# Performance work log

Hardware: AMD Instinct MI355X
Metric: run time of the kernel (lower is better)

## Reference

```python
import jax, jax.numpy as jnp
import numpy as np

N_NODES = 100000
N_EDGES = 1600000
IN_CH = 128
HID = 128
OUT_DIM = 1
N_LAYERS = 3
N_GRAPHS = 512


def setup_inputs() -> dict:
    key = jax.random.key(0)
    ks = jax.random.split(key, 12)
    x = jax.random.normal(ks[0], (N_NODES, IN_CH), dtype=jnp.float32)
    edge_index = jax.random.randint(ks[1], (2, N_EDGES), 0, N_NODES, dtype=jnp.int64)
    batch = jnp.sort(jax.random.randint(ks[2], (N_NODES,), 0, N_GRAPHS, dtype=jnp.int64))
    # GCNConv weights (glorot) and biases; layer 0: in->hid, rest hid->hid (all 128x128 here)
    def glorot(k, fan_in, fan_out):
        lim = jnp.sqrt(6.0 / (fan_in + fan_out)).astype(jnp.float32)
        return jax.random.uniform(k, (fan_in, fan_out), jnp.float32, -lim, lim)
    Ws = jnp.stack([glorot(ks[3 + i], IN_CH if i == 0 else HID, HID) for i in range(N_LAYERS)])
    bs = jnp.zeros((N_LAYERS, HID), dtype=jnp.float32)
    head_w = glorot(ks[8], HID, OUT_DIM)  # stored as [hid, out] == head_weight.T
    head_b = jnp.zeros((OUT_DIM,), dtype=jnp.float32)
    return {"x": x, "edge_index": edge_index, "batch": batch,
            "Ws": Ws, "bs": bs, "head_w": head_w, "head_b": head_b}


def _gcn_norm(edge_index, n_nodes):
    # PyG gcn_norm: add self-loops, deg over dst, norm = d^-1/2[src]*d^-1/2[dst]
    loops = jnp.arange(n_nodes, dtype=edge_index.dtype)
    src = jnp.concatenate([edge_index[0], loops])
    dst = jnp.concatenate([edge_index[1], loops])
    deg = jax.ops.segment_sum(jnp.ones_like(dst, dtype=jnp.float32), dst, num_segments=n_nodes)
    dinv = jnp.where(deg > 0, jax.lax.rsqrt(deg), 0.0)
    norm = dinv[src] * dinv[dst]
    return src, dst, norm


def reference(x, edge_index, batch, Ws, bs, head_w, head_b):
    n = x.shape[0]
    src, dst, norm = _gcn_norm(edge_index, n)
    h = x.astype(jnp.float32)
    for i in range(N_LAYERS):
        t = h @ Ws[i]                                   # [N, hid]
        msg = t[src] * norm[:, None]                    # gather + scale [E+N, hid]
        h = jax.ops.segment_sum(msg, dst, num_segments=n) + bs[i]
        h = jax.nn.relu(h)                              # dropout p=0 -> identity
    g = jax.ops.segment_sum(h, batch, num_segments=N_GRAPHS)  # global_add_pool
    out = g @ head_w + head_b                           # [G, 1]
    return out.reshape(-1)                              # squeeze out_dim==1
```

## Files before the change

kernel.cpp:

```cpp
#include <hip/hip_runtime.h>

#define NN 100000
#define NE 1600000
#define CH 128
#define NG 512
#define NL 3
#define BSZ 512
#define NBUK ((NN + BSZ - 1) / BSZ)
#define TILE 4096

typedef short bf8 __attribute__((ext_vector_type(8)));
typedef float f4 __attribute__((ext_vector_type(4)));
typedef unsigned int u32x4 __attribute__((ext_vector_type(4)));
typedef unsigned short u16;
typedef unsigned int u32;

__device__ __forceinline__ long long ld_idx(const void* p, long long i, bool is64) {
    return is64 ? ((const long long*)p)[i] : (long long)((const int*)p)[i];
}
__device__ __forceinline__ u16 f2bf(float f) {
    u32 u = __float_as_uint(f);
    u += 0x7fffu + ((u >> 16) & 1u);
    return (u16)(u >> 16);
}
__device__ __forceinline__ float bflo(u32 v) { return __uint_as_float(v << 16); }
__device__ __forceinline__ float bfhi(u32 v) { return __uint_as_float(v & 0xffff0000u); }

__global__ void k_zero(int* bcnt, int* flags) {
    int i = blockIdx.x * blockDim.x + threadIdx.x;
    if (i < NBUK) bcnt[i] = 0;
    if (i < 2) flags[i] = 0;
}

__global__ void k_detect(const int* __restrict__ ei32, const int* __restrict__ b32, int* flags) {
    int acc_e = 0, acc_b = 0;
    long long stride = (long long)gridDim.x * blockDim.x;
    long long t0 = (long long)blockIdx.x * blockDim.x + threadIdx.x;
    for (long long i = t0; i < (1 << 18); i += stride) acc_e |= ei32[2 * i + 1];
    for (long long i = t0; i < NN / 2; i += stride) acc_b |= b32[2 * i + 1];
    if (acc_e) atomicOr(&flags[0], 1);
    if (acc_b) atomicOr(&flags[1], 1);
}


__global__ __launch_bounds__(256) void k_hist(const void* __restrict__ ei,
                                              const int* __restrict__ flags,
                                              int* __restrict__ bcnt) {
    __shared__ int cnt[NBUK];
    int tid = threadIdx.x;
    long long e0 = (long long)blockIdx.x * TILE;
    bool is64 = (flags[0] == 0);
    for (int b = tid; b < NBUK; b += 256) cnt[b] = 0;
    __syncthreads();
#pragma unroll
    for (int k = 0; k < 16; ++k) {
        long long e = e0 + tid + k * 256;
        if (e < NE) {
            int d = (int)ld_idx(ei, NE + e, is64);
            atomicAdd(&cnt[d >> 9], 1);
        }
    }
    __syncthreads();
    for (int b = tid; b < NBUK; b += 256)
        if (cnt[b]) atomicAdd(&bcnt[b], cnt[b]);
}

__global__ __launch_bounds__(256) void k_bscan(const int* __restrict__ bcnt,
                                               int* __restrict__ gbase,
                                               int* __restrict__ gcur,
                                               int* __restrict__ rowptr) {
    __shared__ int ws4[4];
    int t = threadIdx.x;
    int v = (t < NBUK) ? bcnt[t] : 0;
    int x = v;
#pragma unroll
    for (int d = 1; d < 64; d <<= 1) {
        int y = __shfl_up(x, d, 64);
        if ((t & 63) >= d) x += y;
    }
    if ((t & 63) == 63) ws4[t >> 6] = x;
    __syncthreads();
    if (t == 0) {
        int s = 0;
#pragma unroll
        for (int w = 0; w < 4; ++w) { int tmp = ws4[w]; ws4[w] = s; s += tmp; }
    }
    __syncthreads();
    int ex = x - v + ws4[t >> 6];
    if (t < NBUK) { gbase[t] = ex; gcur[t] = ex; }
    if (t == NBUK - 1) gbase[NBUK] = ex + v;
    if (t == 0) rowptr[NN] = NE;
}

__global__ __launch_bounds__(256) void k_bin(const void* __restrict__ ei,
                                             const int* __restrict__ flags,
                                             int* __restrict__ gcur,
                                             u32* __restrict__ bin) {
    __shared__ u32 stag[TILE];
    __shared__ int cnt[NBUK], loff[NBUK], lcur[NBUK], gb_s[NBUK];
    int tid = threadIdx.x;
    long long e0 = (long long)blockIdx.x * TILE;
    bool is64 = (flags[0] == 0);

    u32 rec[16];
    int bk[16];
#pragma unroll
    for (int k = 0; k < 16; ++k) {
        long long e = e0 + tid + k * 256;
        if (e < NE) {
            int s = (int)ld_idx(ei, e, is64);
            int d = (int)ld_idx(ei, NE + e, is64);
            rec[k] = ((u32)s << 9) | (u32)(d & (BSZ - 1));
            bk[k] = d >> 9;
        } else bk[k] = -1;
    }
    for (int b = tid; b < NBUK; b += 256) { cnt[b] = 0; lcur[b] = 0; }
    __syncthreads();
#pragma unroll
    for (int k = 0; k < 16; ++k)
        if (bk[k] >= 0) atomicAdd(&cnt[bk[k]], 1);
    __syncthreads();
    if (tid == 0) {
        int run = 0;
        for (int b = 0; b < NBUK; ++b) { loff[b] = run; run += cnt[b]; }
    }
    __syncthreads();
    if (tid < NBUK && cnt[tid] > 0) gb_s[tid] = atomicAdd(&gcur[tid], cnt[tid]);
    __syncthreads();
#pragma unroll
    for (int k = 0; k < 16; ++k)
        if (bk[k] >= 0) {
            int pos = loff[bk[k]] + atomicAdd(&lcur[bk[k]], 1);
            stag[pos] = rec[k];
        }
    __syncthreads();
    int wv = tid >> 6, lane = tid & 63;
    for (int b = wv; b < NBUK; b += 4) {
        int n = cnt[b];
        int gb = (n > 0) ? gb_s[b] : 0;
        int lo = loff[b];
        for (int j = lane; j < n; j += 64) bin[gb + j] = stag[lo + j];
    }
}

__global__ __launch_bounds__(512) void k_fillc(const u32* __restrict__ bin,
                                               const int* __restrict__ gbase,
                                               int* __restrict__ rowptr,
                                               float* __restrict__ dinv,
                                               u32* __restrict__ csr) {
    __shared__ int cnt[BSZ];
    __shared__ int lcur[BSZ];
    __shared__ int wsum[8];
    int b = blockIdx.x, tid = threadIdx.x;
    int gb = gbase[b], ge = gbase[b + 1];
    cnt[tid] = 0;
    __syncthreads();
    for (int i = gb + tid; i < ge; i += BSZ)
        atomicAdd(&cnt[bin[i] & (BSZ - 1)], 1);
    __syncthreads();
    int v = cnt[tid];
    int x = v;
#pragma unroll
    for (int d = 1; d < 64; d <<= 1) {
        int y = __shfl_up(x, d, 64);
        if ((tid & 63) >= d) x += y;
    }
    if ((tid & 63) == 63) wsum[tid >> 6] = x;
    __syncthreads();
    if (tid == 0) {
        int s = 0;
#pragma unroll
        for (int w = 0; w < 8; ++w) { int tmp = wsum[w]; wsum[w] = s; s += tmp; }
    }
    __syncthreads();
    int off = gb + x - v + wsum[tid >> 6];
    int node = b * BSZ + tid;
    if (node < NN) {
        rowptr[node] = off;
        dinv[node] = rsqrtf((float)v + 1.0f);
    }
    lcur[tid] = off;
    __syncthreads();
    for (int i = gb + tid; i < ge; i += BSZ) {
        u32 rec = bin[i];
        int pos = atomicAdd(&lcur[rec & (BSZ - 1)], 1);
        csr[pos] = rec >> 9;
    }
}

__global__ void k_cvt(const float* __restrict__ x, u16* __restrict__ xb,
                      const float* __restrict__ Ws, u16* __restrict__ Wt) {
    long long i = ((long long)blockIdx.x * blockDim.x + threadIdx.x) * 4;
    const long long NX = (long long)NN * CH;
    if (i < NX) {
        float4 v = *(const float4*)(x + i);
        ushort4 o;
        o.x = f2bf(v.x); o.y = f2bf(v.y); o.z = f2bf(v.z); o.w = f2bf(v.w);
        *(ushort4*)(xb + i) = o;
    } else {
        int j = (int)(i - NX);
        if (j >= NL * CH * CH) return;
        int l = j >> 14, c = (j >> 7) & 127, k = j & 127;
        ushort4 o;
        o.x = f2bf(Ws[(l << 14) + ((k + 0) << 7) + c]);
        o.y = f2bf(Ws[(l << 14) + ((k + 1) << 7) + c]);
        o.z = f2bf(Ws[(l << 14) + ((k + 2) << 7) + c]);
        o.w = f2bf(Ws[(l << 14) + ((k + 3) << 7) + c]);
        *(ushort4*)(Wt + j) = o;
    }
}

__global__ __launch_bounds__(256) void k_mm(const u16* __restrict__ A,
                                            const u16* __restrict__ Wt,
                                            u16* __restrict__ out) {
    int tid = threadIdx.x;
    int lane = tid & 63;
    int wv = tid >> 6;
    int rbase = blockIdx.x * 128 + wv * 32;
    int lm = lane & 15;
    int lk = (lane >> 4) << 3;

    f4 acc[2][8];
#pragma unroll
    for (int m = 0; m < 2; ++m)
#pragma unroll
        for (int n = 0; n < 8; ++n) acc[m][n] = (f4){0.f, 0.f, 0.f, 0.f};

    int r0 = rbase + lm;      if (r0 >= NN) r0 = NN - 1;
    int r1 = rbase + 16 + lm; if (r1 >= NN) r1 = NN - 1;

#pragma unroll
    for (int kk = 0; kk < 4; ++kk) {
        int ko = kk * 32 + lk;
        bf8 a0 = *(const bf8*)(A + (size_t)r0 * CH + ko);
        bf8 a1 = *(const bf8*)(A + (size_t)r1 * CH + ko);
#pragma unroll
        for (int n = 0; n < 8; ++n) {
            bf8 b = *(const bf8*)(Wt + (n * 16 + lm) * CH + ko);
            acc[0][n] = __builtin_amdgcn_mfma_f32_16x16x32_bf16(a0, b, acc[0][n], 0, 0, 0);
            acc[1][n] = __builtin_amdgcn_mfma_f32_16x16x32_bf16(a1, b, acc[1][n], 0, 0, 0);
        }
    }

#pragma unroll
    for (int m = 0; m < 2; ++m) {
        int rb = rbase + m * 16 + (lane >> 4) * 4;
#pragma unroll
        for (int r = 0; r < 4; ++r) {
            int row = rb + r;
            if (row < NN) {
#pragma unroll
                for (int n = 0; n < 8; ++n)
                    out[(size_t)row * CH + n * 16 + lm] = f2bf(acc[m][n][r]);
            }
        }
    }
}

#define ACC8W(v, w) \
    acc[0] = fmaf(bflo(v[0]), w, acc[0]); acc[1] = fmaf(bfhi(v[0]), w, acc[1]); \
    acc[2] = fmaf(bflo(v[1]), w, acc[2]); acc[3] = fmaf(bfhi(v[1]), w, acc[3]); \
    acc[4] = fmaf(bflo(v[2]), w, acc[4]); acc[5] = fmaf(bfhi(v[2]), w, acc[5]); \
    acc[6] = fmaf(bflo(v[3]), w, acc[6]); acc[7] = fmaf(bfhi(v[3]), w, acc[7]);

__global__ __launch_bounds__(256) void k_aggr(const u16* __restrict__ t,
                                              const int* __restrict__ rowptr,
                                              const u32* __restrict__ csr,
                                              const float* __restrict__ dinv,
                                              const float* __restrict__ b,
                                              u16* __restrict__ h,
                                              const float* __restrict__ hw,
                                              float* __restrict__ partial) {
    int node = blockIdx.x * 16 + (threadIdx.x >> 4);
    if (node >= NN) return;
    int l16 = threadIdx.x & 15;
    int c8 = l16 << 3;
    const u32x4* tp = (const u32x4*)t;

    int beg = rowptr[node], end = rowptr[node + 1];
    float dn = dinv[node];
    float acc[8];
#pragma unroll
    for (int k = 0; k < 8; ++k) acc[k] = 0.f;

    int j = beg;
    for (; j + 4 <= end; j += 4) {
        int s0 = (int)csr[j], s1 = (int)csr[j + 1];
        int s2 = (int)csr[j + 2], s3 = (int)csr[j + 3];
        float w0 = dinv[s0], w1 = dinv[s1], w2 = dinv[s2], w3 = dinv[s3];
        u32x4 v0 = tp[s0 * 16 + l16];
        u32x4 v1 = tp[s1 * 16 + l16];
        u32x4 v2 = tp[s2 * 16 + l16];
        u32x4 v3 = tp[s3 * 16 + l16];
        ACC8W(v0, w0); ACC8W(v1, w1); ACC8W(v2, w2); ACC8W(v3, w3);
    }
    for (; j < end; ++j) {
        int s = (int)csr[j];
        float w = dinv[s];
        u32x4 v = tp[s * 16 + l16];
        ACC8W(v, w);
    }

    u32x4 sv = tp[node * 16 + l16];
    float4 b0 = *(const float4*)(b + c8);
    float4 b1 = *(const float4*)(b + c8 + 4);
    float r[8];
    r[0] = fmaxf(fmaf(fmaf(bflo(sv[0]), dn, acc[0]), dn, b0.x), 0.f);
    r[1] = fmaxf(fmaf(fmaf(bfhi(sv[0]), dn, acc[1]), dn, b0.y), 0.f);
    r[2] = fmaxf(fmaf(fmaf(bflo(sv[1]), dn, acc[2]), dn, b0.z), 0.f);
    r[3] = fmaxf(fmaf(fmaf(bfhi(sv[1]), dn, acc[3]), dn, b0.w), 0.f);
    r[4] = fmaxf(fmaf(fmaf(bflo(sv[2]), dn, acc[4]), dn, b1.x), 0.f);
    r[5] = fmaxf(fmaf(fmaf(bfhi(sv[2]), dn, acc[5]), dn, b1.y), 0.f);
    r[6] = fmaxf(fmaf(fmaf(bflo(sv[3]), dn, acc[6]), dn, b1.z), 0.f);
    r[7] = fmaxf(fmaf(fmaf(bfhi(sv[3]), dn, acc[7]), dn, b1.w), 0.f);

    if (hw) {
        float4 w0 = *(const float4*)(hw + c8);
        float4 w1 = *(const float4*)(hw + c8 + 4);
        float d = r[0] * w0.x + r[1] * w0.y + r[2] * w0.z + r[3] * w0.w
                + r[4] * w1.x + r[5] * w1.y + r[6] * w1.z + r[7] * w1.w;
#pragma unroll
        for (int off = 8; off > 0; off >>= 1) d += __shfl_xor(d, off);
        if (l16 == 0) partial[node] = d;
    } else {
        u32x4 o;
        o[0] = ((u32)f2bf(r[1]) << 16) | (u32)f2bf(r[0]);
        o[1] = ((u32)f2bf(r[3]) << 16) | (u32)f2bf(r[2]);
        o[2] = ((u32)f2bf(r[5]) << 16) | (u32)f2bf(r[4]);
        o[3] = ((u32)f2bf(r[7]) << 16) | (u32)f2bf(r[6]);
        ((u32x4*)h)[node * 16 + l16] = o;
    }
}


__device__ __forceinline__ int lbound(const void* bt, bool is64, int target) {
    int lo = 0, hi = NN;
    while (lo < hi) {
        int mid = (lo + hi) >> 1;
        long long v = ld_idx(bt, mid, is64);
        if (v < (long long)target) lo = mid + 1; else hi = mid;
    }
    return lo;
}

__global__ __launch_bounds__(256) void k_head(const float* __restrict__ partial,
                                              const void* __restrict__ batch,
                                              const int* __restrict__ flags,
                                              const float* __restrict__ hb,
                                              float* __restrict__ out) {
    int g = blockIdx.x * 4 + (threadIdx.x >> 6);
    if (g >= NG) return;
    int lane = threadIdx.x & 63;
    bool is64 = (flags[1] == 0);
    int lo = lbound(batch, is64, g);
    int hi = lbound(batch, is64, g + 1);
    float s = 0.f;
    for (int i = lo + lane; i < hi; i += 64) s += partial[i];
#pragma unroll
    for (int off = 32; off > 0; off >>= 1) s += __shfl_down(s, off);
    if (lane == 0) out[g] = s + hb[0];
}

extern "C" void kernel_launch(void* const* d_in, const int* in_sizes, int n_in,
                              void* d_out, int out_size, void* d_ws, size_t ws_size,
                              hipStream_t stream) {
    const float* x  = (const float*)d_in[0];
    const void*  ei = d_in[1];
    const void*  bt = d_in[2];
    const float* Ws = (const float*)d_in[3];
    const float* bs = (const float*)d_in[4];
    const float* hw = (const float*)d_in[5];
    const float* hb = (const float*)d_in[6];
    float* out = (float*)d_out;

    char* ws = (char*)d_ws;
    size_t p = 0;
    auto alloc = [&](size_t bytes) { size_t r = p; p += (bytes + 255) & ~(size_t)255; return r; };
    size_t o_flags  = alloc(256);
    size_t o_dinv   = alloc((size_t)NN * 4);
    size_t o_rowptr = alloc((size_t)(NN + 1) * 4);
    size_t o_bcnt   = alloc((size_t)NBUK * 4);
    size_t o_gbase  = alloc((size_t)(NBUK + 1) * 4);
    size_t o_gcur   = alloc((size_t)NBUK * 4);
    size_t o_part   = alloc((size_t)NN * 4);
    size_t o_bin    = alloc((size_t)NE * 4);
    size_t o_csr    = alloc((size_t)NE * 4);
    size_t o_xb     = alloc((size_t)NN * CH * 2);
    size_t o_tb     = alloc((size_t)NN * CH * 2);
    size_t o_hb     = alloc((size_t)NN * CH * 2);
    size_t o_wt     = alloc((size_t)NL * CH * CH * 2);
    (void)ws_size;

    int*   flags  = (int*)(ws + o_flags);
    float* dinv   = (float*)(ws + o_dinv);
    int*   rowptr = (int*)(ws + o_rowptr);
    int*   bcnt   = (int*)(ws + o_bcnt);
    int*   gbase  = (int*)(ws + o_gbase);
    int*   gcur   = (int*)(ws + o_gcur);
    float* part   = (float*)(ws + o_part);
    u32*   bin    = (u32*)(ws + o_bin);
    u32*   csr    = (u32*)(ws + o_csr);
    u16*   xb     = (u16*)(ws + o_xb);
    u16*   tb     = (u16*)(ws + o_tb);
    u16*   hbuf   = (u16*)(ws + o_hb);
    u16*   Wt     = (u16*)(ws + o_wt);

    k_zero<<<1, 256, 0, stream>>>(bcnt, flags);
    k_detect<<<256, 256, 0, stream>>>((const int*)ei, (const int*)bt, flags);
    k_hist<<<(NE + TILE - 1) / TILE, 256, 0, stream>>>(ei, flags, bcnt);
    k_bscan<<<1, 256, 0, stream>>>(bcnt, gbase, gcur, rowptr);
    k_bin<<<(NE + TILE - 1) / TILE, 256, 0, stream>>>(ei, flags, gcur, bin);
    k_fillc<<<NBUK, BSZ, 0, stream>>>(bin, gbase, rowptr, dinv, csr);

    long long ncv = (long long)NN * CH / 4 + NL * CH * CH / 4;
    k_cvt<<<(int)((ncv + 255) / 256), 256, 0, stream>>>(x, xb, Ws, Wt);

    const u16* hin = xb;
    for (int l = 0; l < NL; ++l) {
        bool last = (l == NL - 1);
        k_mm<<<(NN + 127) / 128, 256, 0, stream>>>(hin, Wt + (size_t)l * CH * CH, tb);
        k_aggr<<<(NN + 15) / 16, 256, 0, stream>>>(tb, rowptr, csr, dinv,
                                                   bs + (size_t)l * CH, hbuf,
                                                   last ? hw : nullptr, part);
        hin = hbuf;
    }

    k_head<<<(NG + 3) / 4, 256, 0, stream>>>(part, bt, flags, hb, out);
}
```

Measured before the change: 373.2 us.

## Fuse fp32-to-bf16 input conversion into first GEMM and unroll aggregation by 8

The separate conversion pass over x is removed. The first-layer matmul now reads fp32 x directly and converts it to bf16 in registers, which saves writing and re-reading a 25.6 MB bf16 copy. Weight conversion moves to a small separate kernel. The aggregation gather loop also gains an 8-way unrolled stage to keep more independent loads in flight, at the cost of more registers.

```diff
diff --git a/kernel.cpp b/kernel.cpp
--- a/kernel.cpp
+++ b/kernel.cpp
@@ -188,31 +188,22 @@
     }
 }
 
-__global__ void k_cvt(const float* __restrict__ x, u16* __restrict__ xb,
-                      const float* __restrict__ Ws, u16* __restrict__ Wt) {
-    long long i = ((long long)blockIdx.x * blockDim.x + threadIdx.x) * 4;
-    const long long NX = (long long)NN * CH;
-    if (i < NX) {
-        float4 v = *(const float4*)(x + i);
-        ushort4 o;
-        o.x = f2bf(v.x); o.y = f2bf(v.y); o.z = f2bf(v.z); o.w = f2bf(v.w);
-        *(ushort4*)(xb + i) = o;
-    } else {
-        int j = (int)(i - NX);
-        if (j >= NL * CH * CH) return;
-        int l = j >> 14, c = (j >> 7) & 127, k = j & 127;
-        ushort4 o;
-        o.x = f2bf(Ws[(l << 14) + ((k + 0) << 7) + c]);
-        o.y = f2bf(Ws[(l << 14) + ((k + 1) << 7) + c]);
-        o.z = f2bf(Ws[(l << 14) + ((k + 2) << 7) + c]);
-        o.w = f2bf(Ws[(l << 14) + ((k + 3) << 7) + c]);
-        *(ushort4*)(Wt + j) = o;
-    }
-}
-
-__global__ __launch_bounds__(256) void k_mm(const u16* __restrict__ A,
-                                            const u16* __restrict__ Wt,
-                                            u16* __restrict__ out) {
+__global__ void k_cvt_w(const float* __restrict__ Ws, u16* __restrict__ Wt) {
+    int j = (blockIdx.x * blockDim.x + threadIdx.x) * 4;
+    if (j >= NL * CH * CH) return;
+    int l = j >> 14, c = (j >> 7) & 127, k = j & 127;
+    ushort4 o;
+    o.x = f2bf(Ws[(l << 14) + ((k + 0) << 7) + c]);
+    o.y = f2bf(Ws[(l << 14) + ((k + 1) << 7) + c]);
+    o.z = f2bf(Ws[(l << 14) + ((k + 2) << 7) + c]);
+    o.w = f2bf(Ws[(l << 14) + ((k + 3) << 7) + c]);
+    *(ushort4*)(Wt + j) = o;
+}
+
+template <int F32IN>
+__global__ __launch_bounds__(256) void k_mm_t(const void* __restrict__ Ain,
+                                              const u16* __restrict__ Wt,
+                                              u16* __restrict__ out) {
     int tid = threadIdx.x;
     int lane = tid & 63;
     int wv = tid >> 6;
@@ -232,8 +223,26 @@
 #pragma unroll
     for (int kk = 0; kk < 4; ++kk) {
         int ko = kk * 32 + lk;
-        bf8 a0 = *(const bf8*)(A + (size_t)r0 * CH + ko);
-        bf8 a1 = *(const bf8*)(A + (size_t)r1 * CH + ko);
+        bf8 a0, a1;
+        if (F32IN) {
+            const float* A = (const float*)Ain;
+            float4 p0 = *(const float4*)(A + (size_t)r0 * CH + ko);
+            float4 q0 = *(const float4*)(A + (size_t)r0 * CH + ko + 4);
+            float4 p1 = *(const float4*)(A + (size_t)r1 * CH + ko);
+            float4 q1 = *(const float4*)(A + (size_t)r1 * CH + ko + 4);
+            a0[0] = (short)f2bf(p0.x); a0[1] = (short)f2bf(p0.y);
+            a0[2] = (short)f2bf(p0.z); a0[3] = (short)f2bf(p0.w);
+            a0[4] = (short)f2bf(q0.x); a0[5] = (short)f2bf(q0.y);
+            a0[6] = (short)f2bf(q0.z); a0[7] = (short)f2bf(q0.w);
+            a1[0] = (short)f2bf(p1.x); a1[1] = (short)f2bf(p1.y);
+            a1[2] = (short)f2bf(p1.z); a1[3] = (short)f2bf(p1.w);
+            a1[4] = (short)f2bf(q1.x); a1[5] = (short)f2bf(q1.y);
+            a1[6] = (short)f2bf(q1.z); a1[7] = (short)f2bf(q1.w);
+        } else {
+            const u16* A = (const u16*)Ain;
+            a0 = *(const bf8*)(A + (size_t)r0 * CH + ko);
+            a1 = *(const bf8*)(A + (size_t)r1 * CH + ko);
+        }
 #pragma unroll
         for (int n = 0; n < 8; ++n) {
             bf8 b = *(const bf8*)(Wt + (n * 16 + lm) * CH + ko);
@@ -284,6 +293,24 @@
     for (int k = 0; k < 8; ++k) acc[k] = 0.f;
 
     int j = beg;
+    for (; j + 8 <= end; j += 8) {
+        int s0 = (int)csr[j],     s1 = (int)csr[j + 1];
+        int s2 = (int)csr[j + 2], s3 = (int)csr[j + 3];
+        int s4 = (int)csr[j + 4], s5 = (int)csr[j + 5];
+        int s6 = (int)csr[j + 6], s7 = (int)csr[j + 7];
+        float w0 = dinv[s0], w1 = dinv[s1], w2 = dinv[s2], w3 = dinv[s3];
+        float w4 = dinv[s4], w5 = dinv[s5], w6 = dinv[s6], w7 = dinv[s7];
+        u32x4 v0 = tp[s0 * 16 + l16];
+        u32x4 v1 = tp[s1 * 16 + l16];
+        u32x4 v2 = tp[s2 * 16 + l16];
+        u32x4 v3 = tp[s3 * 16 + l16];
+        u32x4 v4 = tp[s4 * 16 + l16];
+        u32x4 v5 = tp[s5 * 16 + l16];
+        u32x4 v6 = tp[s6 * 16 + l16];
+        u32x4 v7 = tp[s7 * 16 + l16];
+        ACC8W(v0, w0); ACC8W(v1, w1); ACC8W(v2, w2); ACC8W(v3, w3);
+        ACC8W(v4, w4); ACC8W(v5, w5); ACC8W(v6, w6); ACC8W(v7, w7);
+    }
     for (; j + 4 <= end; j += 4) {
         int s0 = (int)csr[j], s1 = (int)csr[j + 1];
         int s2 = (int)csr[j + 2], s3 = (int)csr[j + 3];
@@ -385,7 +412,6 @@
     size_t o_part   = alloc((size_t)NN * 4);
     size_t o_bin    = alloc((size_t)NE * 4);
     size_t o_csr    = alloc((size_t)NE * 4);
-    size_t o_xb     = alloc((size_t)NN * CH * 2);
     size_t o_tb     = alloc((size_t)NN * CH * 2);
     size_t o_hb     = alloc((size_t)NN * CH * 2);
     size_t o_wt     = alloc((size_t)NL * CH * CH * 2);
@@ -400,7 +426,6 @@
     float* part   = (float*)(ws + o_part);
     u32*   bin    = (u32*)(ws + o_bin);
     u32*   csr    = (u32*)(ws + o_csr);
-    u16*   xb     = (u16*)(ws + o_xb);
     u16*   tb     = (u16*)(ws + o_tb);
     u16*   hbuf   = (u16*)(ws + o_hb);
     u16*   Wt     = (u16*)(ws + o_wt);
@@ -411,18 +436,19 @@
     k_bscan<<<1, 256, 0, stream>>>(bcnt, gbase, gcur, rowptr);
     k_bin<<<(NE + TILE - 1) / TILE, 256, 0, stream>>>(ei, flags, gcur, bin);
     k_fillc<<<NBUK, BSZ, 0, stream>>>(bin, gbase, rowptr, dinv, csr);
-
-    long long ncv = (long long)NN * CH / 4 + NL * CH * CH / 4;
-    k_cvt<<<(int)((ncv + 255) / 256), 256, 0, stream>>>(x, xb, Ws, Wt);
-
-    const u16* hin = xb;
+    k_cvt_w<<<(NL * CH * CH / 4 + 255) / 256, 256, 0, stream>>>(Ws, Wt);
+
+    const void* hin = (const void*)x;
     for (int l = 0; l < NL; ++l) {
         bool last = (l == NL - 1);
-        k_mm<<<(NN + 127) / 128, 256, 0, stream>>>(hin, Wt + (size_t)l * CH * CH, tb);
+        if (l == 0)
+            k_mm_t<1><<<(NN + 127) / 128, 256, 0, stream>>>(hin, Wt, tb);
+        else
+            k_mm_t<0><<<(NN + 127) / 128, 256, 0, stream>>>(hin, Wt + (size_t)l * CH * CH, tb);
         k_aggr<<<(NN + 15) / 16, 256, 0, stream>>>(tb, rowptr, csr, dinv,
                                                    bs + (size_t)l * CH, hbuf,
                                                    last ? hw : nullptr, part);
-        hin = hbuf;
+        hin = (const void*)hbuf;
     }
 
     k_head<<<(NG + 3) / 4, 256, 0, stream>>>(part, bt, flags, hb, out);
```

Result: no change. 367.1 us (-1.6%).
